# Kernel optimization log

Hardware: AMD Instinct MI355X
Metric: run time of the kernel (lower is better)

The kernel has to match this reference:

```python
import jax, jax.numpy as jnp
import numpy as np

B, S, E, F = 8, 1024, 1024, 4096
EPS = 1e-12

def _layer_norm(x, gamma, beta):
    mu = jnp.mean(x, axis=-1, keepdims=True)
    var = jnp.mean(jnp.square(x - mu), axis=-1, keepdims=True)
    return (x - mu) / jnp.sqrt(var + EPS) * gamma + beta

def setup_inputs() -> dict:
    key = jax.random.key(0)
    ks = jax.random.split(key, 16)
    sE = 1.0 / np.sqrt(E)
    sF = 1.0 / np.sqrt(F)
    return {
        'hidden_states': jax.random.normal(ks[0], (B, S, E), jnp.float32),
        'Wq': jax.random.normal(ks[1], (E, E), jnp.float32) * sE,
        'bq': jnp.zeros((E,), jnp.float32),
        'Wk': jax.random.normal(ks[2], (E, E), jnp.float32) * sE,
        'bk': jnp.zeros((E,), jnp.float32),
        'Wv': jax.random.normal(ks[3], (E, E), jnp.float32) * sE,
        'bv': jnp.zeros((E,), jnp.float32),
        'Wd': jax.random.normal(ks[4], (E, E), jnp.float32) * sE,
        'bd': jnp.zeros((E,), jnp.float32),
        'g1': jnp.ones((E,), jnp.float32),
        'b1': jnp.zeros((E,), jnp.float32),
        'Wi': jax.random.normal(ks[5], (E, F), jnp.float32) * sE,
        'bi': jnp.zeros((F,), jnp.float32),
        'Wo': jax.random.normal(ks[6], (F, E), jnp.float32) * sF,
        'bo': jnp.zeros((E,), jnp.float32),
        'g2': jnp.ones((E,), jnp.float32),
        'b2': jnp.zeros((E,), jnp.float32),
    }

def reference(hidden_states, Wq, bq, Wk, bk, Wv, bv, Wd, bd, g1, b1, Wi, bi, Wo, bo, g2, b2):
    x = hidden_states
    q = x @ Wq + bq                     # [B,S,E]
    k = x @ Wk + bk
    v = x @ Wv + bv
    scores = jnp.einsum('bqe,bke->bqk', q, k) / jnp.sqrt(jnp.float32(E))
    attn_w = jax.nn.softmax(scores, axis=-1)
    attn_out = jnp.einsum('bqk,bke->bqe', attn_w, v)
    # add_norm 1 (dropout = identity in eval)
    h1 = _layer_norm(attn_out @ Wd + bd + x, g1, b1)
    ff = jax.nn.gelu(h1 @ Wi + bi, approximate=False)   # forward_act
    # NOTE: original code's second add_norm uses forward_act (pre out_dense),
    # applying out_dense inside add_norm -> LN(out_dense(ff) + h1)
    out = _layer_norm(ff @ Wo + bo + h1, g2, b2)
    return out
```

## Files before the change

kernel.cpp:

```cpp
#include <hip/hip_runtime.h>
#include <math.h>


typedef __bf16 bf16;
typedef __attribute__((ext_vector_type(8))) __bf16 bf16x8;
typedef __attribute__((ext_vector_type(4))) __bf16 bf16x4;
typedef __attribute__((ext_vector_type(4))) float f32x4;

#define BM 128
#define BN 128
#define BK 64
#define SCS 140

__device__ __forceinline__ void async_cp16(const bf16* g, bf16* l) {
    __builtin_amdgcn_global_load_lds((__attribute__((address_space(1))) void*)(g),
                                     (__attribute__((address_space(3))) void*)(l),
                                     16, 0, 0);
}

__device__ __forceinline__ float gelu_fast(float x) {
    float u = x * x;
    float y = 1.5957691216f * x * fmaf(0.044715f, u, 1.0f);
    float e = __expf(-y);
    return x * __builtin_amdgcn_rcpf(1.0f + e);
}

__device__ __forceinline__ float load_dual(const void* p, long long i, int f32) {
    return f32 ? ((const float*)p)[i] : (float)((const bf16*)p)[i];
}


__global__ void diag_init(const void* x, int* dflag)
{
    const int t = threadIdx.x;
    const bf16* xb = (const bf16*)x;
    float a = (float)xb[2 * t];
    float b = (float)xb[2 * t + 1];
    auto wild = [](float v) -> bool {
        float af = fabsf(v);
        return !(af <= 3.0e38f) || af > 1.0e3f || (v != 0.0f && af < 1.0e-8f);
    };
    unsigned long long ba = __ballot(wild(a));
    unsigned long long bb = __ballot(wild(b));
    if (t == 0) *dflag = (__popcll(ba) + __popcll(bb) > 16) ? 1 : 0;
}

__global__ void sentinel_small(float* out) { out[0] = 2048.0f; }


__global__ __launch_bounds__(256)
void convert_vec4(const void* src, bf16* dst, long long n4, const int* dflag)
{
    const int f32 = *dflag;
    long long i = (long long)blockIdx.x * 256 + threadIdx.x;
    if (i >= n4) return;
    bf16x4 o;
    if (f32) {
        f32x4 v = ((const f32x4*)src)[i];
        #pragma unroll
        for (int j = 0; j < 4; j++) o[j] = (bf16)v[j];
    } else {
        o = ((const bf16x4*)src)[i];
    }
    ((bf16x4*)dst)[i] = o;
}

struct SmallPtrs { const void* p[10]; };

__global__ __launch_bounds__(256)
void convert_small(SmallPtrs sp, bf16* dst, const int* dflag)
{
    const int f32 = *dflag;
    const int idx = blockIdx.x * 256 + threadIdx.x;
    if (idx >= 13312) return;
    const int seg = idx >> 10;
    float v;
    if (seg < 9) v = load_dual(sp.p[seg], idx & 1023, f32);
    else         v = load_dual(sp.p[9], idx - 9216, f32);
    dst[idx] = (bf16)v;
}

__global__ __launch_bounds__(256)
void transpose_dual(const void* in, bf16* out, int R, int C, const int* dflag)
{
    __shared__ bf16 tile[32][33];
    const int f32 = *dflag;
    const int c0 = blockIdx.x * 32, r0 = blockIdx.y * 32;
    const int tx = threadIdx.x, ty = threadIdx.y;
    #pragma unroll
    for (int i = 0; i < 32; i += 8)
        tile[ty + i][tx] = (bf16)load_dual(in, (long long)(r0 + ty + i) * C + (c0 + tx), f32);
    __syncthreads();
    #pragma unroll
    for (int i = 0; i < 32; i += 8)
        out[(long long)(c0 + ty + i) * R + (r0 + tx)] = tile[tx][ty + i];
}

__global__ __launch_bounds__(256)
void transpose_b(const bf16* __restrict__ in, bf16* __restrict__ out, int R, int C)
{
    __shared__ bf16 tile[32][33];
    const long long z = (long long)blockIdx.z * (long long)R * C;
    const int c0 = blockIdx.x * 32, r0 = blockIdx.y * 32;
    const int tx = threadIdx.x, ty = threadIdx.y;
    #pragma unroll
    for (int i = 0; i < 32; i += 8)
        tile[ty + i][tx] = in[z + (long long)(r0 + ty + i) * C + (c0 + tx)];
    __syncthreads();
    #pragma unroll
    for (int i = 0; i < 32; i += 8)
        out[z + (long long)(c0 + ty + i) * R + (r0 + tx)] = tile[tx][ty + i];
}

template<int ACT, int HAS_BIAS, int HAS_RES, int OUT_F32>
__global__ __launch_bounds__(512)
void gemm_bt(const bf16* __restrict__ A, const bf16* __restrict__ Bt,
             const bf16* __restrict__ bias, const bf16* __restrict__ res,
             void* __restrict__ Cout, int M, int N, int K, float scale,
             long long bsA, long long bsB, long long bsC, long long bsBias)
{
    __shared__ __align__(16) char smem[65536];
    float* sC = (float*)smem;

    const int tid  = threadIdx.x;
    const int lane = tid & 63;
    const int wave = tid >> 6;
    const int pw   = wave & 3;
    const int wm   = pw >> 1;
    const int wn   = pw & 1;
    const bool producer = (wave >= 4);
    const int m0   = blockIdx.y * BM;
    const int n0   = blockIdx.x * BN;
    const long long zA = (long long)blockIdx.z * bsA;
    const long long zB = (long long)blockIdx.z * bsB;
    const long long zC = (long long)blockIdx.z * bsC;
    const bf16* biasz = HAS_BIAS ? (bias + (long long)blockIdx.z * bsBias) : nullptr;
    const int nIter = K >> 6;

    f32x4 acc[4][4];
    const bf16* gA[4]; const bf16* gB[4]; int lo[4];

    if (producer) {
        #pragma unroll
        for (int j = 0; j < 4; j++) {
            const int ci  = j * 256 + pw * 64 + lane;
            const int row = ci >> 3;
            const int c8  = ((ci & 7) ^ (row & 7)) * 8;
            gA[j] = A + zA + (long long)(m0 + row) * K + c8;
            gB[j] = Bt + zB + (long long)(n0 + row) * K + c8;
            lo[j] = (j * 256 + pw * 64) * 8;
        }
        bf16* dA = (bf16*)smem;
        bf16* dB = (bf16*)(smem + 16384);
        #pragma unroll
        for (int j = 0; j < 4; j++) {
            async_cp16(gA[j], dA + lo[j]);
            async_cp16(gB[j], dB + lo[j]);
            gA[j] += BK; gB[j] += BK;
        }
    } else {
        const f32x4 zf = {0.f, 0.f, 0.f, 0.f};
        #pragma unroll
        for (int i = 0; i < 4; i++)
            #pragma unroll
            for (int j = 0; j < 4; j++) acc[i][j] = zf;
    }
    __syncthreads();

    const int fr   = lane & 15;
    const int x0   = (lane >> 4) ^ (fr & 7);
    const int arow = wm * 64 + fr;
    const int brow = wn * 64 + fr;

    for (int kt = 0; kt < nIter; ++kt) {
        if (producer) {
            if (kt + 1 < nIter) {
                const int bo = ((kt + 1) & 1) ? 32768 : 0;
                bf16* dA = (bf16*)(smem + bo);
                bf16* dB = (bf16*)(smem + bo + 16384);
                #pragma unroll
                for (int j = 0; j < 4; j++) {
                    async_cp16(gA[j], dA + lo[j]);
                    async_cp16(gB[j], dB + lo[j]);
                    gA[j] += BK; gB[j] += BK;
                }
            }
        } else {
            const int bo = (kt & 1) ? 32768 : 0;
            const bf16* sAk = (const bf16*)(smem + bo);
            const bf16* sBk = (const bf16*)(smem + bo + 16384);
            #pragma unroll
            for (int s = 0; s < 2; s++) {
                const int xo = (x0 ^ (s << 2)) * 8;
                bf16x8 afr[4], bfr[4];
                #pragma unroll
                for (int mi = 0; mi < 4; mi++) afr[mi] = *(const bf16x8*)(sAk + (arow + mi * 16) * 64 + xo);
                #pragma unroll
                for (int ni = 0; ni < 4; ni++) bfr[ni] = *(const bf16x8*)(sBk + (brow + ni * 16) * 64 + xo);
                #pragma unroll
                for (int mi = 0; mi < 4; mi++)
                    #pragma unroll
                    for (int ni = 0; ni < 4; ni++)
                        acc[mi][ni] = __builtin_amdgcn_mfma_f32_16x16x32_bf16(afr[mi], bfr[ni], acc[mi][ni], 0, 0, 0);
            }
        }
        __syncthreads();
    }

    const int q4 = lane >> 4;
    for (int h = 0; h < 2; h++) {
        __syncthreads();
        if (!producer && wm == h) {
            #pragma unroll
            for (int mi = 0; mi < 4; mi++)
                #pragma unroll
                for (int r = 0; r < 4; r++) {
                    const int lr = mi * 16 + q4 * 4 + r;
                    #pragma unroll
                    for (int ni = 0; ni < 4; ni++)
                        sC[lr * SCS + wn * 64 + ni * 16 + fr] = acc[mi][ni][r];
                }
        }
        __syncthreads();
        const int lr = tid >> 3;
        const int cb = (tid & 7) * 16;
        const long long grow  = m0 + h * 64 + lr;
        const long long gbase = zC + grow * (long long)N + (n0 + cb);
        const float* srow = sC + lr * SCS + cb;
        #pragma unroll
        for (int g = 0; g < 2; g++) {
            f32x4 v0 = *(const f32x4*)(srow + g * 8);
            f32x4 v1 = *(const f32x4*)(srow + g * 8 + 4);
            float vv[8] = {v0[0], v0[1], v0[2], v0[3], v1[0], v1[1], v1[2], v1[3]};
            if constexpr (HAS_BIAS) {
                bf16x8 bb = *(const bf16x8*)(biasz + n0 + cb + g * 8);
                #pragma unroll
                for (int j = 0; j < 8; j++) vv[j] = vv[j] * scale + (float)bb[j];
            } else {
                #pragma unroll
                for (int j = 0; j < 8; j++) vv[j] *= scale;
            }
            if constexpr (ACT == 1) {
                #pragma unroll
                for (int j = 0; j < 8; j++) vv[j] = gelu_fast(vv[j]);
            }
            if constexpr (HAS_RES) {
                bf16x8 rr = *(const bf16x8*)(res + gbase + g * 8);
                #pragma unroll
                for (int j = 0; j < 8; j++) vv[j] += (float)rr[j];
            }
            if constexpr (OUT_F32) {
                f32x4 o0 = {vv[0], vv[1], vv[2], vv[3]};
                f32x4 o1 = {vv[4], vv[5], vv[6], vv[7]};
                *(f32x4*)((float*)Cout + gbase + g * 8)     = o0;
                *(f32x4*)((float*)Cout + gbase + g * 8 + 4) = o1;
            } else {
                bf16x8 o;
                #pragma unroll
                for (int j = 0; j < 8; j++) o[j] = (bf16)vv[j];
                *(bf16x8*)((bf16*)Cout + gbase + g * 8) = o;
            }
        }
    }
}

template<int ACT, int HAS_BIAS, int HAS_RES, int OUT_F32, int SPLITK>
__global__ __launch_bounds__(512, 2)
void gemm256(const bf16* __restrict__ A, const bf16* __restrict__ Bt,
             const bf16* __restrict__ bias, const bf16* __restrict__ res,
             void* __restrict__ Cout, void* __restrict__ Cout2,
             int M, int N, int K, int ldk, float scale,
             long long bsB, long long bsC, long long bsBias)
{
    __shared__ __align__(16) char smem[131072];

    const int tid  = threadIdx.x;
    const int lane = tid & 63;
    const int wave = tid >> 6;
    const int wm   = wave >> 2;
    const int wn   = wave & 3;

    const int gx  = N >> 8;
    const int nwg = gx * (M >> 8);
    int wg = blockIdx.x;
    {
        const int q = nwg >> 3, r = nwg & 7;
        const int xcd = wg & 7, lid = wg >> 3;
        wg = (xcd < r ? xcd * (q + 1) : r * (q + 1) + (xcd - r) * q) + lid;
    }
    const int bx = wg % gx, by = wg / gx;
    const int m0 = by << 8, n0 = bx << 8;
    const int zi = blockIdx.y;

    const bf16* Ab = A  + (SPLITK ? (long long)zi * K : 0);
    const bf16* Bb = Bt + (SPLITK ? (long long)zi * K : (long long)zi * bsB);
    const bool  bon = HAS_BIAS && (!SPLITK || zi == 0);
    const bool  ron = HAS_RES  && (!SPLITK || zi == 0);
    const bf16* biasz = HAS_BIAS ? (bias + (SPLITK ? 0 : (long long)zi * bsBias)) : nullptr;
    const long long coff = SPLITK ? 0 : (long long)zi * bsC;
    char* const Cb = (char*)((SPLITK && zi) ? Cout2 : Cout);

    int soff[2];
    #pragma unroll
    for (int qq = 0; qq < 2; qq++) {
        const int g   = (wave * 2 + qq) * 64 + lane;
        const int rp  = g >> 3, sub = g & 7;
        const int row = rp * 2 + (sub >> 2);
        const int cc  = (sub & 3) ^ (rp & 3);
        soff[qq] = row * ldk + cc * 8;
    }
    const bf16* aS0 = Ab + (long long)m0 * ldk + soff[0];
    const bf16* aS1 = Ab + (long long)m0 * ldk + soff[1];
    const bf16* bS0 = Bb + (long long)n0 * ldk + soff[0];
    const bf16* bS1 = Bb + (long long)n0 * ldk + soff[1];
    char* const ldsW = smem + wave * 2048;

    const int fr = lane & 15, chk = lane >> 4;
    const int ra  = wm * 128 + fr;
    const int aRd = (ra >> 1) * 128 + (ra & 1) * 64 + ((chk ^ ((ra >> 1) & 3)) * 16);
    const int rb  = wn * 64 + fr;
    const int bRd = 32768 + (rb >> 1) * 128 + (rb & 1) * 64 + ((chk ^ ((rb >> 1) & 3)) * 16);

    unsigned aAddr[4], bAddr[4];
    {
        const unsigned sm3 = (unsigned)(size_t)(__attribute__((address_space(3))) char*)smem;
        #pragma unroll
        for (int cb = 0; cb < 2; cb++)
            #pragma unroll
            for (int s = 0; s < 2; s++) {
                aAddr[cb * 2 + s] = sm3 + cb * 65536 + s * 16384 + aRd;
                bAddr[cb * 2 + s] = sm3 + cb * 65536 + s * 16384 + bRd;
            }
    }

#define DSR(d, b, imm) \
    asm volatile("ds_read_b128 %0, %1 offset:%c2" : "=v"(d) : "v"(b), "i"(imm))
#define RDA(set, idx, mh) do { \
    DSR(set[0], aAddr[idx], ((mh) * 4 + 0) * 1024); \
    DSR(set[1], aAddr[idx], ((mh) * 4 + 1) * 1024); \
    DSR(set[2], aAddr[idx], ((mh) * 4 + 2) * 1024); \
    DSR(set[3], aAddr[idx], ((mh) * 4 + 3) * 1024); \
} while (0)
#define RDB(set, idx) do { \
    DSR(set[0], bAddr[idx], 0); \
    DSR(set[1], bAddr[idx], 1024); \
    DSR(set[2], bAddr[idx], 2048); \
    DSR(set[3], bAddr[idx], 3072); \
} while (0)
#define STG(buf, mat, h, t) do { \
    char* _d = ldsW + (buf) * 65536 + (mat) * 32768 + (h) * 16384; \
    const int _ko = (t) * 64 + (h) * 32; \
    async_cp16(((mat) ? bS0 : aS0) + _ko, (bf16*)_d); \
    async_cp16(((mat) ? bS1 : aS1) + _ko, (bf16*)(_d + 1024)); \
} while (0)
#define IF_STG(c, buf, mat, h, t) do { if (c) STG(buf, mat, h, t); } while (0)
#define BARR __builtin_amdgcn_s_barrier()
#define SB0  __builtin_amdgcn_sched_barrier(0)
#define LGKM0 asm volatile("s_waitcnt lgkmcnt(0)")
#define VM_WAIT(c) do { \
    if (c) asm volatile("s_waitcnt vmcnt(6)"); \
    else   asm volatile("s_waitcnt vmcnt(0)"); \
} while (0)
#define MMA(ASET, BSET, mh) do { \
    __builtin_amdgcn_s_setprio(1); \
    _Pragma("unroll") \
    for (int _j = 0; _j < 4; _j++) { \
        acc[(mh) * 4 + 0][_j] = __builtin_amdgcn_mfma_f32_16x16x32_bf16(ASET[0], BSET[_j], acc[(mh) * 4 + 0][_j], 0, 0, 0); \
        acc[(mh) * 4 + 1][_j] = __builtin_amdgcn_mfma_f32_16x16x32_bf16(ASET[1], BSET[_j], acc[(mh) * 4 + 1][_j], 0, 0, 0); \
        acc[(mh) * 4 + 2][_j] = __builtin_amdgcn_mfma_f32_16x16x32_bf16(ASET[2], BSET[_j], acc[(mh) * 4 + 2][_j], 0, 0, 0); \
        acc[(mh) * 4 + 3][_j] = __builtin_amdgcn_mfma_f32_16x16x32_bf16(ASET[3], BSET[_j], acc[(mh) * 4 + 3][_j], 0, 0, 0); \
    } \
    __builtin_amdgcn_s_setprio(0); \
} while (0)

    const int NT = K >> 6, NI = NT >> 1;

    STG(0, 1, 0, 0); STG(0, 0, 0, 0); STG(0, 1, 1, 0); STG(0, 0, 1, 0);
    STG(1, 1, 0, 1); STG(1, 0, 0, 1); STG(1, 1, 1, 1);

    f32x4 acc[8][4];
    {
        const f32x4 zf = {0.f, 0.f, 0.f, 0.f};
        #pragma unroll
        for (int i = 0; i < 8; i++)
            #pragma unroll
            for (int j = 0; j < 4; j++) acc[i][j] = zf;
    }
    bf16x8 avA[4], avB[4], bvA[4], bvB[4];

    asm volatile("s_waitcnt vmcnt(6)");
    BARR;

    for (int it = 0; it < NI; ++it) {
        const int o = 2 * it + 1, e2 = 2 * it + 2, o2 = 2 * it + 3;
        const bool se = e2 < NT, so = o2 < NT;
        RDA(avA, 0, 0); RDB(bvA, 0);
        STG(1, 0, 1, o);
        BARR; LGKM0; SB0;
        RDA(avB, 0, 1);
        SB0;
        MMA(avA, bvA, 0);
        BARR;
        IF_STG(se, 0, 1, 0, e2);
        BARR; LGKM0; SB0;
        RDA(avA, 1, 0); RDB(bvB, 1);
        SB0;
        MMA(avB, bvA, 1);
        BARR;
        IF_STG(se, 0, 0, 0, e2);
        BARR; LGKM0; SB0;
        RDA(avB, 1, 1);
        SB0;
        MMA(avA, bvB, 0);
        BARR;
        IF_STG(se, 0, 1, 1, e2);
        BARR; LGKM0; SB0;
        MMA(avB, bvB, 1);
        SB0;
        VM_WAIT(se);
        BARR;
        RDA(avA, 2, 0); RDB(bvA, 2);
        IF_STG(se, 0, 0, 1, e2);
        BARR; LGKM0; SB0;
        RDA(avB, 2, 1);
        SB0;
        MMA(avA, bvA, 0);
        BARR;
        IF_STG(so, 1, 1, 0, o2);
        BARR; LGKM0; SB0;
        RDA(avA, 3, 0); RDB(bvB, 3);
        SB0;
        MMA(avB, bvA, 1);
        BARR;
        IF_STG(so, 1, 0, 0, o2);
        BARR; LGKM0; SB0;
        RDA(avB, 3, 1);
        SB0;
        MMA(avA, bvB, 0);
        BARR;
        IF_STG(so, 1, 1, 1, o2);
        BARR; LGKM0; SB0;
        MMA(avB, bvB, 1);
        SB0;
        VM_WAIT(so);
        BARR;
    }
#undef MMA
#undef VM_WAIT
#undef LGKM0
#undef SB0
#undef BARR
#undef IF_STG
#undef STG
#undef RDB
#undef RDA
#undef DSR

    float* sC = (float*)smem;
    const int q4 = lane >> 4;
    const int lr = tid >> 3;
    const int c0 = (tid & 7) * 4;
    const long long Nll = N;
    #pragma unroll
    for (int p = 0; p < 4; p++) {
        __syncthreads();
        if (wm == (p >> 1)) {
            #pragma unroll
            for (int i = 0; i < 4; i++) {
                const int fi = (p & 1) * 4 + i;
                #pragma unroll
                for (int r = 0; r < 4; r++) {
                    const int row = i * 16 + q4 * 4 + r;
                    #pragma unroll
                    for (int j = 0; j < 4; j++)
                        sC[row * 260 + wn * 64 + j * 16 + fr] = acc[fi][j][r];
                }
            }
        }
        __syncthreads();
        const long long grow = m0 + p * 64 + lr;
        const long long gb = grow * Nll + n0;
        const float* srow = sC + lr * 260;
        #pragma unroll
        for (int g = 0; g < 8; g++) {
            const int col = c0 + g * 32;
            f32x4 v = *(const f32x4*)(srow + col);
            float vv[4] = {v[0], v[1], v[2], v[3]};
            if (bon) {
                bf16x4 bb = *(const bf16x4*)(biasz + n0 + col);
                #pragma unroll
                for (int j = 0; j < 4; j++) vv[j] = vv[j] * scale + (float)bb[j];
            } else {
                #pragma unroll
                for (int j = 0; j < 4; j++) vv[j] *= scale;
            }
            if constexpr (ACT == 1) {
                #pragma unroll
                for (int j = 0; j < 4; j++) vv[j] = gelu_fast(vv[j]);
            }
            if (ron) {
                bf16x4 rr = *(const bf16x4*)(res + gb + col);
                #pragma unroll
                for (int j = 0; j < 4; j++) vv[j] += (float)rr[j];
            }
            if constexpr (OUT_F32) {
                f32x4 o4 = {vv[0], vv[1], vv[2], vv[3]};
                *(f32x4*)((float*)Cb + coff + gb + col) = o4;
            } else {
                bf16x4 o4;
                #pragma unroll
                for (int j = 0; j < 4; j++) o4[j] = (bf16)vv[j];
                *(bf16x4*)((bf16*)Cb + coff + gb + col) = o4;
            }
        }
    }
}


__global__ __launch_bounds__(256)
void softmax_inplace(bf16* __restrict__ P, int N)
{
    const long long row = blockIdx.x;
    bf16* p = P + row * (long long)N;
    const int t = threadIdx.x;
    bf16x4 xin = *(const bf16x4*)(p + t * 4);
    float xs[4];
    #pragma unroll
    for (int i = 0; i < 4; i++) xs[i] = (float)xin[i];

    float m = fmaxf(fmaxf(xs[0], xs[1]), fmaxf(xs[2], xs[3]));
    #pragma unroll
    for (int off = 32; off > 0; off >>= 1) m = fmaxf(m, __shfl_xor(m, off, 64));
    __shared__ float red[4];
    if ((t & 63) == 0) red[t >> 6] = m;
    __syncthreads();
    m = fmaxf(fmaxf(red[0], red[1]), fmaxf(red[2], red[3]));

    float e[4], s = 0.f;
    #pragma unroll
    for (int i = 0; i < 4; i++) { e[i] = __expf(xs[i] - m); s += e[i]; }
    #pragma unroll
    for (int off = 32; off > 0; off >>= 1) s += __shfl_xor(s, off, 64);
    __shared__ float red2[4];
    if ((t & 63) == 0) red2[t >> 6] = s;
    __syncthreads();
    s = red2[0] + red2[1] + red2[2] + red2[3];
    const float inv = 1.f / s;

    bf16x4 o;
    #pragma unroll
    for (int i = 0; i < 4; i++) o[i] = (bf16)(e[i] * inv);
    *(bf16x4*)(p + t * 4) = o;
}

template<int IN_MODE, int OUT_F32>
__global__ __launch_bounds__(256)
void layernorm_rows(const void* __restrict__ Z, const void* __restrict__ Z2,
                    const bf16* __restrict__ g, const bf16* __restrict__ b,
                    void* __restrict__ outp, int N)
{
    const long long row = blockIdx.x;
    const int t = threadIdx.x;
    float xv[4];
    if constexpr (IN_MODE >= 1) {
        f32x4 zin = *(const f32x4*)((const float*)Z + row * (long long)N + t * 4);
        #pragma unroll
        for (int i = 0; i < 4; i++) xv[i] = zin[i];
        if constexpr (IN_MODE == 2) {
            f32x4 z2 = *(const f32x4*)((const float*)Z2 + row * (long long)N + t * 4);
            #pragma unroll
            for (int i = 0; i < 4; i++) xv[i] += z2[i];
        }
    } else {
        bf16x4 zin = *(const bf16x4*)((const bf16*)Z + row * (long long)N + t * 4);
        #pragma unroll
        for (int i = 0; i < 4; i++) xv[i] = (float)zin[i];
    }

    float s = xv[0] + xv[1] + xv[2] + xv[3];
    #pragma unroll
    for (int off = 32; off > 0; off >>= 1) s += __shfl_xor(s, off, 64);
    __shared__ float r1[4];
    if ((t & 63) == 0) r1[t >> 6] = s;
    __syncthreads();
    const float mu = (r1[0] + r1[1] + r1[2] + r1[3]) * (1.f / 1024.f);

    float d[4];
    float sq = 0.f;
    #pragma unroll
    for (int i = 0; i < 4; i++) { d[i] = xv[i] - mu; sq += d[i] * d[i]; }
    #pragma unroll
    for (int off = 32; off > 0; off >>= 1) sq += __shfl_xor(sq, off, 64);
    __shared__ float r2[4];
    if ((t & 63) == 0) r2[t >> 6] = sq;
    __syncthreads();
    const float var = (r2[0] + r2[1] + r2[2] + r2[3]) * (1.f / 1024.f);
    const float rstd = rsqrtf(var + 1e-12f);

    bf16x4 gv = *(const bf16x4*)(g + t * 4);
    bf16x4 bv = *(const bf16x4*)(b + t * 4);
    if constexpr (OUT_F32) {
        f32x4 o;
        #pragma unroll
        for (int i = 0; i < 4; i++)
            o[i] = d[i] * rstd * (float)gv[i] + (float)bv[i];
        *(f32x4*)((float*)outp + row * (long long)N + t * 4) = o;
    } else {
        bf16x4 o;
        #pragma unroll
        for (int i = 0; i < 4; i++)
            o[i] = (bf16)(d[i] * rstd * (float)gv[i] + (float)bv[i]);
        *(bf16x4*)((bf16*)outp + row * (long long)N + t * 4) = o;
    }
}


extern "C" void kernel_launch(void* const* d_in, const int* in_sizes, int n_in,
                              void* d_out, int out_size, void* d_ws, size_t ws_size,
                              hipStream_t stream)
{
    (void)in_sizes; (void)n_in; (void)out_size;

    const void* x  = d_in[0];
    const void* Wq = d_in[1];  const void* bq = d_in[2];
    const void* Wk = d_in[3];  const void* bk = d_in[4];
    const void* Wv = d_in[5];  const void* bv = d_in[6];
    const void* Wd = d_in[7];  const void* bd = d_in[8];
    const void* g1 = d_in[9];  const void* b1 = d_in[10];
    const void* Wi = d_in[11]; const void* bi = d_in[12];
    const void* Wo = d_in[13]; const void* bo = d_in[14];
    const void* g2 = d_in[15]; const void* b2 = d_in[16];

    const int Bb = 8, S = 1024, E = 1024, F = 4096;
    const int M = Bb * S;
    const long long SE = (long long)S * E, SS = (long long)S * S;
    const long long ME = (long long)M * E;

    char* ws = (char*)d_ws;
    const size_t MB = 1024ull * 1024ull;
    int*  dflag = (int*)(ws + 0);
    bf16* small = (bf16*)(ws + 64 * 1024);
    bf16* bq_c = small + 0 * 1024;
    bf16* bd_c = small + 3 * 1024;
    bf16* g1_c = small + 4 * 1024;
    bf16* b1_c = small + 5 * 1024;
    bf16* g2_c = small + 6 * 1024;
    bf16* b2_c = small + 7 * 1024;
    bf16* bo_c = small + 8 * 1024;
    bf16* bi_c = small + 9216;
    bf16* WoT  = (bf16*)(ws + 1 * MB);
    bf16* WiT  = (bf16*)(ws + 9 * MB);
    bf16* WqT  = (bf16*)(ws + 17 * MB);
    bf16* WkT  = (bf16*)(ws + 19 * MB);
    bf16* WvT  = (bf16*)(ws + 21 * MB);
    bf16* WdT  = (bf16*)(ws + 23 * MB);
    bf16* xb   = (bf16*)(ws + 25 * MB);
    float* out = (float*)d_out;

    diag_init<<<1, 64, 0, stream>>>(x, dflag);

    if (ws_size < 70 * MB) { sentinel_small<<<1, 1, 0, stream>>>(out); return; }

    SmallPtrs sp;
    sp.p[0] = bq; sp.p[1] = bk; sp.p[2] = bv; sp.p[3] = bd; sp.p[4] = g1;
    sp.p[5] = b1; sp.p[6] = g2; sp.p[7] = b2; sp.p[8] = bo; sp.p[9] = bi;
    convert_small<<<52, 256, 0, stream>>>(sp, small, dflag);
    convert_vec4<<<8192, 256, 0, stream>>>(x, xb, ME / 4, dflag);

    const dim3 tb(32, 8, 1);
    transpose_dual<<<dim3(E/32, E/32), tb, 0, stream>>>(Wq, WqT, E, E, dflag);
    transpose_dual<<<dim3(E/32, E/32), tb, 0, stream>>>(Wk, WkT, E, E, dflag);
    transpose_dual<<<dim3(E/32, E/32), tb, 0, stream>>>(Wv, WvT, E, E, dflag);
    transpose_dual<<<dim3(E/32, E/32), tb, 0, stream>>>(Wd, WdT, E, E, dflag);
    transpose_dual<<<dim3(F/32, E/32), tb, 0, stream>>>(Wi, WiT, E, F, dflag);
    transpose_dual<<<dim3(E/32, F/32), tb, 0, stream>>>(Wo, WoT, F, E, dflag);

    if (ws_size >= 121 * MB) {
        bf16* qkv  = (bf16*)(ws + 41 * MB);
        bf16* q    = qkv;
        bf16* k    = qkv + ME;
        bf16* v    = qkv + 2 * ME;
        bf16* vT   = (bf16*)(ws + 89 * MB);
        bf16* P    = (bf16*)(ws + 73 * MB);
        bf16* attn = (bf16*)(ws + 41 * MB);
        bf16* z1   = (bf16*)(ws + 57 * MB);
        bf16* h1   = (bf16*)(ws + 41 * MB);
        bf16* ff   = (bf16*)(ws + 57 * MB);
        float* z2a = (float*)(ws + 9 * MB);
        float* z2b = (float*)(ws + 89 * MB);

        gemm256<0,1,0,0,0><<<dim3((E/256)*(M/256), 3), 512, 0, stream>>>(
            xb, WqT, bq_c, nullptr, qkv, nullptr, M, E, E, E, 1.f,
            (long long)E * E, ME, E);
        transpose_b<<<dim3(E/32, S/32, Bb), tb, 0, stream>>>(v, vT, S, E);
        gemm_bt<0,0,0,0><<<dim3(8, 8, Bb), 512, 0, stream>>>(
            q, k, nullptr, nullptr, P, S, S, E, 0.03125f, SE, SE, SS, 0);
        softmax_inplace<<<M, 256, 0, stream>>>(P, S);
        gemm_bt<0,0,0,0><<<dim3(8, 8, Bb), 512, 0, stream>>>(
            P, vT, nullptr, nullptr, attn, S, E, S, 1.f, SS, SE, SE, 0);
        gemm_bt<0,1,1,0><<<dim3(8, 64), 512, 0, stream>>>(
            attn, WdT, bd_c, xb, z1, M, E, E, 1.f, 0, 0, 0, 0);
        layernorm_rows<0,0><<<M, 256, 0, stream>>>(z1, nullptr, g1_c, b1_c, h1, E);
        gemm256<1,1,0,0,0><<<dim3((F/256)*(M/256), 1), 512, 0, stream>>>(
            h1, WiT, bi_c, nullptr, ff, nullptr, M, F, E, E, 1.f, 0, 0, 0);
        gemm256<0,1,1,1,1><<<dim3((E/256)*(M/256), 2), 512, 0, stream>>>(
            ff, WoT, bo_c, h1, z2a, z2b, M, E, F / 2, F, 1.f, 0, 0, 0);
        layernorm_rows<2,1><<<M, 256, 0, stream>>>(z2a, z2b, g2_c, b2_c, out, E);
    } else {
        bf16* qkv_b = (bf16*)(ws + 41 * MB);
        bf16* q_b   = qkv_b;
        bf16* k_b   = qkv_b + SE;
        bf16* v_b   = qkv_b + 2 * SE;
        bf16* vT_b  = (bf16*)(ws + 47 * MB);
        bf16* P_b   = (bf16*)(ws + 49 * MB);
        bf16* at_b  = (bf16*)(ws + 51 * MB);
        bf16* z1_b  = (bf16*)(ws + 53 * MB);
        bf16* h1_b  = (bf16*)(ws + 55 * MB);
        bf16* ff_b  = (bf16*)(ws + 57 * MB);
        bf16* z2_b  = (bf16*)(ws + 65 * MB);

        for (int b = 0; b < Bb; b++) {
            const bf16* x_b = xb + (long long)b * SE;
            gemm_bt<0,1,0,0><<<dim3(8, 8, 3), 512, 0, stream>>>(
                x_b, WqT, bq_c, nullptr, qkv_b, S, E, E, 1.f, 0, (long long)E * E, SE, E);
            transpose_b<<<dim3(E/32, S/32), tb, 0, stream>>>(v_b, vT_b, S, E);
            gemm_bt<0,0,0,0><<<dim3(8, 8), 512, 0, stream>>>(
                q_b, k_b, nullptr, nullptr, P_b, S, S, E, 0.03125f, 0, 0, 0, 0);
            softmax_inplace<<<S, 256, 0, stream>>>(P_b, S);
            gemm_bt<0,0,0,0><<<dim3(8, 8), 512, 0, stream>>>(
                P_b, vT_b, nullptr, nullptr, at_b, S, E, S, 1.f, 0, 0, 0, 0);
            gemm_bt<0,1,1,0><<<dim3(8, 8), 512, 0, stream>>>(
                at_b, WdT, bd_c, x_b, z1_b, S, E, E, 1.f, 0, 0, 0, 0);
            layernorm_rows<0,0><<<S, 256, 0, stream>>>(z1_b, nullptr, g1_c, b1_c, h1_b, E);
            gemm_bt<1,1,0,0><<<dim3(32, 8), 512, 0, stream>>>(
                h1_b, WiT, bi_c, nullptr, ff_b, S, F, E, 1.f, 0, 0, 0, 0);
            gemm_bt<0,1,1,0><<<dim3(8, 8), 512, 0, stream>>>(
                ff_b, WoT, bo_c, h1_b, z2_b, S, E, F, 1.f, 0, 0, 0, 0);
            layernorm_rows<0,1><<<S, 256, 0, stream>>>(z2_b, nullptr, g2_c, b2_c, out + (long long)b * SE, E);
        }
    }
}
```

Measured before the change: 507.5 us.

## Restructure GEMM LDS layout to full-K rows with XOR swizzle and reorder MFMA stages

Changes the shared-memory tile layout of the 256x256 GEMM from half-K split planes to full 64-wide K rows with an XOR swizzle on 16-byte slots. Global-to-LDS async copies and the ds_read addressing are rewritten to match. The B fragment for all 64 K is now loaded once per buffer into eight registers, and the MFMA stage sequence and vmcnt waits are reordered. The goal is fewer LDS bank conflicts and fewer B reloads. The cost is more live registers and a different copy/compute interleave.

Result: no change. 501.7 us (-1.1%).

```diff
diff --git a/kernel.cpp b/kernel.cpp
--- a/kernel.cpp
+++ b/kernel.cpp
@@ -300,83 +300,79 @@
     const long long coff = SPLITK ? 0 : (long long)zi * bsC;
     char* const Cb = (char*)((SPLITK && zi) ? Cout2 : Cout);
 
-    int soff[2];
-    #pragma unroll
-    for (int qq = 0; qq < 2; qq++) {
-        const int g   = (wave * 2 + qq) * 64 + lane;
-        const int rp  = g >> 3, sub = g & 7;
-        const int row = rp * 2 + (sub >> 2);
-        const int cc  = (sub & 3) ^ (rp & 3);
-        soff[qq] = row * ldk + cc * 8;
-    }
-    const bf16* aS0 = Ab + (long long)m0 * ldk + soff[0];
-    const bf16* aS1 = Ab + (long long)m0 * ldk + soff[1];
-    const bf16* bS0 = Bb + (long long)n0 * ldk + soff[0];
-    const bf16* bS1 = Bb + (long long)n0 * ldk + soff[1];
-    char* const ldsW = smem + wave * 2048;
+    const int rg0 = wave * 16 + (lane >> 3);
+    const int cg0 = (lane & 7) ^ (lane >> 3);
+    const bf16* aSrc[2]; const bf16* bSrc[2];
+    #pragma unroll
+    for (int h = 0; h < 2; h++) {
+        aSrc[h] = Ab + (long long)(m0 + h * 128 + rg0) * ldk + cg0 * 8;
+        bSrc[h] = Bb + (long long)(n0 + h * 128 + rg0) * ldk + cg0 * 8;
+    }
+    const int sq8 = 8 * ldk;
 
     const int fr = lane & 15, chk = lane >> 4;
-    const int ra  = wm * 128 + fr;
-    const int aRd = (ra >> 1) * 128 + (ra & 1) * 64 + ((chk ^ ((ra >> 1) & 3)) * 16);
-    const int rb  = wn * 64 + fr;
-    const int bRd = 32768 + (rb >> 1) * 128 + (rb & 1) * 64 + ((chk ^ ((rb >> 1) & 3)) * 16);
-
     unsigned aAddr[4], bAddr[4];
     {
         const unsigned sm3 = (unsigned)(size_t)(__attribute__((address_space(3))) char*)smem;
         #pragma unroll
         for (int cb = 0; cb < 2; cb++)
             #pragma unroll
-            for (int s = 0; s < 2; s++) {
-                aAddr[cb * 2 + s] = sm3 + cb * 65536 + s * 16384 + aRd;
-                bAddr[cb * 2 + s] = sm3 + cb * 65536 + s * 16384 + bRd;
+            for (int kk = 0; kk < 2; kk++) {
+                const unsigned slot = (unsigned)(((kk * 4 + chk) ^ (fr & 7)) * 16);
+                aAddr[cb * 2 + kk] = sm3 + cb * 65536 + wm * 16384
+                                   + fr * 128 + slot;
+                bAddr[cb * 2 + kk] = sm3 + cb * 65536 + 32768 + (wn >> 1) * 16384
+                                   + ((wn & 1) * 64 + fr) * 128 + slot;
             }
     }
 
 #define DSR(d, b, imm) \
     asm volatile("ds_read_b128 %0, %1 offset:%c2" : "=v"(d) : "v"(b), "i"(imm))
-#define RDA(set, idx, mh) do { \
-    DSR(set[0], aAddr[idx], ((mh) * 4 + 0) * 1024); \
-    DSR(set[1], aAddr[idx], ((mh) * 4 + 1) * 1024); \
-    DSR(set[2], aAddr[idx], ((mh) * 4 + 2) * 1024); \
-    DSR(set[3], aAddr[idx], ((mh) * 4 + 3) * 1024); \
+#define RDA4(set, cb, q) do { \
+    DSR(set[0], aAddr[(cb) * 2 + 0], (q) * 4096); \
+    DSR(set[1], aAddr[(cb) * 2 + 1], (q) * 4096); \
+    DSR(set[2], aAddr[(cb) * 2 + 0], (q) * 4096 + 2048); \
+    DSR(set[3], aAddr[(cb) * 2 + 1], (q) * 4096 + 2048); \
 } while (0)
-#define RDB(set, idx) do { \
-    DSR(set[0], bAddr[idx], 0); \
-    DSR(set[1], bAddr[idx], 1024); \
-    DSR(set[2], bAddr[idx], 2048); \
-    DSR(set[3], bAddr[idx], 3072); \
+#define RDB8(cb) do { \
+    DSR(bv[0], bAddr[(cb) * 2 + 0], 0);    DSR(bv[1], bAddr[(cb) * 2 + 1], 0); \
+    DSR(bv[2], bAddr[(cb) * 2 + 0], 2048); DSR(bv[3], bAddr[(cb) * 2 + 1], 2048); \
+    DSR(bv[4], bAddr[(cb) * 2 + 0], 4096); DSR(bv[5], bAddr[(cb) * 2 + 1], 4096); \
+    DSR(bv[6], bAddr[(cb) * 2 + 0], 6144); DSR(bv[7], bAddr[(cb) * 2 + 1], 6144); \
 } while (0)
 #define STG(buf, mat, h, t) do { \
-    char* _d = ldsW + (buf) * 65536 + (mat) * 32768 + (h) * 16384; \
-    const int _ko = (t) * 64 + (h) * 32; \
-    async_cp16(((mat) ? bS0 : aS0) + _ko, (bf16*)_d); \
-    async_cp16(((mat) ? bS1 : aS1) + _ko, (bf16*)(_d + 1024)); \
+    bf16* _d = (bf16*)(smem + (buf) * 65536 + (mat) * 32768 + (h) * 16384 + wave * 2048); \
+    const bf16* _s = ((mat) ? bSrc[h] : aSrc[h]) + (t) * 64; \
+    async_cp16(_s, _d); \
+    async_cp16(_s + sq8, _d + 512); \
 } while (0)
 #define IF_STG(c, buf, mat, h, t) do { if (c) STG(buf, mat, h, t); } while (0)
 #define BARR __builtin_amdgcn_s_barrier()
 #define SB0  __builtin_amdgcn_sched_barrier(0)
 #define LGKM0 asm volatile("s_waitcnt lgkmcnt(0)")
 #define VM_WAIT(c) do { \
-    if (c) asm volatile("s_waitcnt vmcnt(6)"); \
+    if (c) asm volatile("s_waitcnt vmcnt(4)"); \
     else   asm volatile("s_waitcnt vmcnt(0)"); \
 } while (0)
-#define MMA(ASET, BSET, mh) do { \
+#define MMA(q, ASET) do { \
     __builtin_amdgcn_s_setprio(1); \
     _Pragma("unroll") \
     for (int _j = 0; _j < 4; _j++) { \
-        acc[(mh) * 4 + 0][_j] = __builtin_amdgcn_mfma_f32_16x16x32_bf16(ASET[0], BSET[_j], acc[(mh) * 4 + 0][_j], 0, 0, 0); \
-        acc[(mh) * 4 + 1][_j] = __builtin_amdgcn_mfma_f32_16x16x32_bf16(ASET[1], BSET[_j], acc[(mh) * 4 + 1][_j], 0, 0, 0); \
-        acc[(mh) * 4 + 2][_j] = __builtin_amdgcn_mfma_f32_16x16x32_bf16(ASET[2], BSET[_j], acc[(mh) * 4 + 2][_j], 0, 0, 0); \
-        acc[(mh) * 4 + 3][_j] = __builtin_amdgcn_mfma_f32_16x16x32_bf16(ASET[3], BSET[_j], acc[(mh) * 4 + 3][_j], 0, 0, 0); \
+        acc[(q) * 2 + 0][_j] = __builtin_amdgcn_mfma_f32_16x16x32_bf16(ASET[0], bv[_j * 2 + 0], acc[(q) * 2 + 0][_j], 0, 0, 0); \
+        acc[(q) * 2 + 1][_j] = __builtin_amdgcn_mfma_f32_16x16x32_bf16(ASET[2], bv[_j * 2 + 0], acc[(q) * 2 + 1][_j], 0, 0, 0); \
+    } \
+    _Pragma("unroll") \
+    for (int _j = 0; _j < 4; _j++) { \
+        acc[(q) * 2 + 0][_j] = __builtin_amdgcn_mfma_f32_16x16x32_bf16(ASET[1], bv[_j * 2 + 1], acc[(q) * 2 + 0][_j], 0, 0, 0); \
+        acc[(q) * 2 + 1][_j] = __builtin_amdgcn_mfma_f32_16x16x32_bf16(ASET[3], bv[_j * 2 + 1], acc[(q) * 2 + 1][_j], 0, 0, 0); \
     } \
     __builtin_amdgcn_s_setprio(0); \
 } while (0)
 
     const int NT = K >> 6, NI = NT >> 1;
 
-    STG(0, 1, 0, 0); STG(0, 0, 0, 0); STG(0, 1, 1, 0); STG(0, 0, 1, 0);
-    STG(1, 1, 0, 1); STG(1, 0, 0, 1); STG(1, 1, 1, 1);
+    STG(0, 0, 0, 0); STG(0, 0, 1, 0); STG(0, 1, 0, 0); STG(0, 1, 1, 0);
+    STG(1, 1, 0, 1); STG(1, 1, 1, 1);
 
     f32x4 acc[8][4];
     {
@@ -386,62 +382,56 @@
             #pragma unroll
             for (int j = 0; j < 4; j++) acc[i][j] = zf;
     }
-    bf16x8 avA[4], avB[4], bvA[4], bvB[4];
-
-    asm volatile("s_waitcnt vmcnt(6)");
+    bf16x8 avA[4], avB[4], bv[8];
+
+    asm volatile("s_waitcnt vmcnt(4)");
     BARR;
 
     for (int it = 0; it < NI; ++it) {
         const int o = 2 * it + 1, e2 = 2 * it + 2, o2 = 2 * it + 3;
         const bool se = e2 < NT, so = o2 < NT;
-        RDA(avA, 0, 0); RDB(bvA, 0);
+        RDB8(0);
+        RDA4(avA, 0, 0);
+        STG(1, 0, 0, o);
+        BARR; LGKM0; SB0;
+        RDA4(avB, 0, 1); SB0;
+        MMA(0, avA);
+        BARR;
         STG(1, 0, 1, o);
         BARR; LGKM0; SB0;
-        RDA(avB, 0, 1);
-        SB0;
-        MMA(avA, bvA, 0);
+        RDA4(avA, 0, 2); SB0;
+        MMA(1, avB);
         BARR;
         IF_STG(se, 0, 1, 0, e2);
         BARR; LGKM0; SB0;
-        RDA(avA, 1, 0); RDB(bvB, 1);
-        SB0;
-        MMA(avB, bvA, 1);
-        BARR;
-        IF_STG(se, 0, 0, 0, e2);
-        BARR; LGKM0; SB0;
-        RDA(avB, 1, 1);
-        SB0;
-        MMA(avA, bvB, 0);
+        RDA4(avB, 0, 3); SB0;
+        MMA(2, avA);
         BARR;
         IF_STG(se, 0, 1, 1, e2);
         BARR; LGKM0; SB0;
-        MMA(avB, bvB, 1);
-        SB0;
+        MMA(3, avB); SB0;
         VM_WAIT(se);
         BARR;
-        RDA(avA, 2, 0); RDB(bvA, 2);
+        RDB8(1);
+        RDA4(avA, 1, 0);
+        IF_STG(se, 0, 0, 0, e2);
+        BARR; LGKM0; SB0;
+        RDA4(avB, 1, 1); SB0;
+        MMA(0, avA);
+        BARR;
         IF_STG(se, 0, 0, 1, e2);
         BARR; LGKM0; SB0;
-        RDA(avB, 2, 1);
-        SB0;
-        MMA(avA, bvA, 0);
+        RDA4(avA, 1, 2); SB0;
+        MMA(1, avB);
         BARR;
         IF_STG(so, 1, 1, 0, o2);
         BARR; LGKM0; SB0;
-        RDA(avA, 3, 0); RDB(bvB, 3);
-        SB0;
-        MMA(avB, bvA, 1);
-        BARR;
-        IF_STG(so, 1, 0, 0, o2);
-        BARR; LGKM0; SB0;
-        RDA(avB, 3, 1);
-        SB0;
-        MMA(avA, bvB, 0);
+        RDA4(avB, 1, 3); SB0;
+        MMA(2, avA);
         BARR;
         IF_STG(so, 1, 1, 1, o2);
         BARR; LGKM0; SB0;
-        MMA(avB, bvB, 1);
-        SB0;
+        MMA(3, avB); SB0;
         VM_WAIT(so);
         BARR;
     }
@@ -452,8 +442,8 @@
 #undef BARR
 #undef IF_STG
 #undef STG
-#undef RDB
-#undef RDA
+#undef RDB8
+#undef RDA4
 #undef DSR
 
     float* sC = (float*)smem;
```
